# Optimization experiments

Hardware: AMD Instinct MI355X
Metric: run time of the kernel (lower is better)

## Reference

```python
import jax, jax.numpy as jnp
import numpy as np

EMBED_DIM = 1024
NUM_HEADS = 16
HEAD_DIM = EMBED_DIM // NUM_HEADS


def setup_inputs() -> dict:
    key = jax.random.key(0)
    ks = jax.random.split(key, 11)
    B, S, D = 2, 2048, EMBED_DIM
    s = 1.0 / np.sqrt(D)
    inp = {
        "query": jax.random.normal(ks[0], (B, S, D), jnp.float32),
        "key": jax.random.normal(ks[1], (B, S, D), jnp.float32),
        "value": jax.random.normal(ks[2], (B, S, D), jnp.float32),
        # torch Linear weights: [out, in]
        "Wq": jax.random.normal(ks[3], (D, D), jnp.float32) * s,
        "bq": jnp.zeros((D,), jnp.float32),
        "Wk": jax.random.normal(ks[4], (D, D), jnp.float32) * s,
        "bk": jnp.zeros((D,), jnp.float32),
        "Wv": jax.random.normal(ks[5], (D, D), jnp.float32) * s,
        "bv": jnp.zeros((D,), jnp.float32),
        "Wo": jax.random.normal(ks[6], (D, D), jnp.float32) * s,
        "bo": jnp.zeros((D,), jnp.float32),
    }
    return inp


def reference(query, key, value, Wq, bq, Wk, bk, Wv, bv, Wo, bo):
    B, Q, D = query.shape
    K = key.shape[1]
    H, Hd = NUM_HEADS, HEAD_DIM
    # NOTE: source divides by scaling = head_dim**-0.5, i.e. multiplies by sqrt(head_dim)
    scaling = float(Hd) ** (-0.5)

    q = (query @ Wq.T + bq).reshape(B, Q, H, Hd).transpose(0, 2, 1, 3)  # [B,H,Q,Hd]
    k = (key @ Wk.T + bk).reshape(B, K, H, Hd).transpose(0, 2, 1, 3)    # [B,H,K,Hd]
    v = (value @ Wv.T + bv).reshape(B, K, H, Hd).transpose(0, 2, 1, 3)  # [B,H,K,Hd]

    scores = jnp.einsum("bhqd,bhkd->bhqk", q, k) / scaling
    attn = jax.nn.softmax(scores, axis=-1)  # dropout=0 (eval)
    out = jnp.einsum("bhqk,bhkd->bhqd", attn, v)
    out = out.transpose(0, 2, 1, 3).reshape(B, Q, D)
    return out @ Wo.T + bo
```

## Files before the change

kernel.cpp:

```cpp
#include <hip/hip_runtime.h>
#include <type_traits>
#include <utility>

#define B_ 2
#define S_ 2048
#define D_ 1024
#define H_ 16
#define HD_ 64
#define KDIM 1024

typedef __attribute__((ext_vector_type(8))) short    s16x8;
typedef __attribute__((ext_vector_type(8))) _Float16 h16x8;
typedef __attribute__((ext_vector_type(4))) float    f32x4;
typedef __attribute__((ext_vector_type(4))) int      i32x4;
typedef __attribute__((ext_vector_type(2))) int      i32x2;

template <typename T, typename = void> struct mfma_takes : std::false_type {};
template <typename T>
struct mfma_takes<T, std::void_t<decltype(__builtin_amdgcn_mfma_f32_16x16x32_f16(
    std::declval<T>(), std::declval<T>(), std::declval<f32x4>(), 0, 0, 0))>>
    : std::true_type {};
using frag8 = std::conditional_t<mfma_takes<h16x8>::value, h16x8, s16x8>;

__device__ __forceinline__ f32x4 mfma_f16(frag8 a, frag8 b, f32x4 c) {
  return __builtin_amdgcn_mfma_f32_16x16x32_f16(a, b, c, 0, 0, 0);
}

__device__ __forceinline__ short f2h(float f) {
  _Float16 h = (_Float16)f;
  short s; __builtin_memcpy(&s, &h, 2);
  return s;
}
__device__ __forceinline__ int pk2h(float a, float b) {
  auto p = __builtin_amdgcn_cvt_pkrtz(a, b);
  int r; __builtin_memcpy(&r, &p, 4); return r;
}
__device__ __forceinline__ frag8 ld_frag(const short* p) {
  return __builtin_bit_cast(frag8, *(const i32x4*)p);
}
__device__ __forceinline__ float fast_exp2(float x) {
  return __builtin_amdgcn_exp2f(x);
}

typedef __attribute__((address_space(1))) const void gvoid;
typedef __attribute__((address_space(3))) void lvoid;
__device__ __forceinline__ void async_copy16(const void* g, void* l) {
  __builtin_amdgcn_global_load_lds((gvoid*)g, (lvoid*)l, 16, 0, 0);
}

#define RAW_BARRIER() asm volatile("s_barrier" ::: "memory")
#define WAITCNT_VM(n) asm volatile("s_waitcnt vmcnt(" #n ")" ::: "memory")

__global__ __launch_bounds__(256)
void conv_all(const float* __restrict__ q, const float* __restrict__ k,
              const float* __restrict__ v, const float* __restrict__ Wq,
              const float* __restrict__ Wk, const float* __restrict__ Wv,
              const float* __restrict__ Wo,
              short* __restrict__ qh, short* __restrict__ kh,
              short* __restrict__ vh, short* __restrict__ wq,
              short* __restrict__ wk, short* __restrict__ wv,
              short* __restrict__ wo) {
  const int blk = blockIdx.x;
  const float* src; short* dst; int base;
  if (blk < 2048)      { src = q;  dst = qh; base = blk; }
  else if (blk < 4096) { src = k;  dst = kh; base = blk - 2048; }
  else if (blk < 6144) { src = v;  dst = vh; base = blk - 4096; }
  else if (blk < 6656) { src = Wq; dst = wq; base = blk - 6144; }
  else if (blk < 7168) { src = Wk; dst = wk; base = blk - 6656; }
  else if (blk < 7680) { src = Wv; dst = wv; base = blk - 7168; }
  else                 { src = Wo; dst = wo; base = blk - 7680; }
  const int i = base * 2048 + threadIdx.x * 8;
  float4 a0 = *(const float4*)(src + i);
  float4 a1 = *(const float4*)(src + i + 4);
  short h[8] = { f2h(a0.x), f2h(a0.y), f2h(a0.z), f2h(a0.w),
                 f2h(a1.x), f2h(a1.y), f2h(a1.z), f2h(a1.w) };
  i32x4 ph; __builtin_memcpy(&ph, h, 16);
  *(i32x4*)(dst + i) = ph;
}

__global__ __launch_bounds__(256, 3)
void gemm_qkv(const short* __restrict__ qh, const short* __restrict__ kh,
              const short* __restrict__ vh, const short* __restrict__ wq,
              const short* __restrict__ wk, const short* __restrict__ wv,
              const float* __restrict__ bq, const float* __restrict__ bk,
              const float* __restrict__ bv, short* __restrict__ Qf,
              short* __restrict__ Kf, short* __restrict__ Vt, float QS) {
  __shared__ short As[2 * 4096];
  __shared__ short Bs[2 * 4096];

  const int blk = blockIdx.x;
  const int bn = blk & 7, g = blk >> 3;
  const int z = g >> 5, bm = g & 31;
  const short* Ap = z == 0 ? qh : z == 1 ? kh : vh;
  const short* Wp = z == 0 ? wq : z == 1 ? wk : wv;
  const float* bias = z == 0 ? bq : z == 1 ? bk : bv;
  short* Out = z == 0 ? Qf : z == 1 ? Kf : Vt;
  const float scale = z == 0 ? QS : 1.0f;
  const int omode = z == 2 ? 2 : 1;

  const int t = threadIdx.x, wave = t >> 6, lane = t & 63;
  const int laneN = lane & 15, quad = lane >> 4;
  const int wm = wave & 1, wn = wave >> 1;

  f32x4 acc[4][4];
#pragma unroll
  for (int i = 0; i < 4; ++i)
#pragma unroll
    for (int j = 0; j < 4; ++j)
#pragma unroll
      for (int r = 0; r < 4; ++r) acc[i][j][r] = 0.f;

  auto stage = [&](int buf, int kk) {
#pragma unroll
    for (int j = 0; j < 2; ++j) {
      const int chunk = j * 256 + t;
      const int row = chunk >> 2;
      const int gg = (chunk & 3) ^ ((row >> 1) & 3);
      async_copy16(Ap + (size_t)(bm * 128 + row) * KDIM + kk + gg * 8,
                   As + buf * 4096 + chunk * 8);
      async_copy16(Wp + (size_t)(bn * 128 + row) * KDIM + kk + gg * 8,
                   Bs + buf * 4096 + chunk * 8);
    }
  };

  stage(0, 0);
  int buf = 0;
  for (int kk = 0; kk < KDIM; kk += 32, buf ^= 1) {
    if (kk + 32 < KDIM) {
      stage(buf ^ 1, kk + 32);
      WAITCNT_VM(4);
    } else {
      WAITCNT_VM(0);
    }
    RAW_BARRIER();

    frag8 aF[4], bF[4];
#pragma unroll
    for (int mi = 0; mi < 4; ++mi) {
      const int row = wm * 64 + mi * 16 + laneN;
      aF[mi] = ld_frag(As + buf * 4096 + row * 32 +
                       ((quad ^ ((row >> 1) & 3)) * 8));
    }
#pragma unroll
    for (int ni = 0; ni < 4; ++ni) {
      const int row = wn * 64 + ni * 16 + laneN;
      bF[ni] = ld_frag(Bs + buf * 4096 + row * 32 +
                       ((quad ^ ((row >> 1) & 3)) * 8));
    }
#pragma unroll
    for (int mi = 0; mi < 4; ++mi)
#pragma unroll
      for (int ni = 0; ni < 4; ++ni)
        acc[mi][ni] = mfma_f16(aF[mi], bF[ni], acc[mi][ni]);
    RAW_BARRIER();
  }

#pragma unroll
  for (int mi = 0; mi < 4; ++mi)
#pragma unroll
    for (int ni = 0; ni < 4; ++ni) {
      const int colg = bn * 128 + wn * 64 + ni * 16 + laneN;
      const float bb = bias[colg];
      if (omode == 2) {
        const int rowg0 = bm * 128 + wm * 64 + mi * 16 + quad * 4;
        const int b = rowg0 >> 11, s0 = rowg0 & 2047;
        const int h = colg >> 6, hd = colg & 63;
        short pk[4];
#pragma unroll
        for (int r = 0; r < 4; ++r) pk[r] = f2h(acc[mi][ni][r] + bb);
        i32x2 w; __builtin_memcpy(&w, pk, 8);
        *(i32x2*)(Vt + (((size_t)(b * H_ + h)) * HD_ + hd) * S_ + s0) = w;
      } else {
#pragma unroll
        for (int r = 0; r < 4; ++r) {
          const int rowg = bm * 128 + wm * 64 + mi * 16 + quad * 4 + r;
          const int b = rowg >> 11, s = rowg & 2047;
          const int h = colg >> 6, hd = colg & 63;
          Out[(((size_t)(b * H_ + h)) * S_ + s) * HD_ + hd] =
              f2h((acc[mi][ni][r] + bb) * scale);
        }
      }
    }
}

__global__ __launch_bounds__(256, 3)
void gemm_out(const short* __restrict__ Ap, const short* __restrict__ Wp,
              const float* __restrict__ bias, float* __restrict__ Out) {
  __shared__ short As[2 * 4096];
  __shared__ short Bs[2 * 2048];
  const int blk = blockIdx.x;
  const int g = blk >> 3;
  const int bn = (blk & 7) * 2 + (g & 1), bm = g >> 1;

  const int t = threadIdx.x, wave = t >> 6, lane = t & 63;
  const int laneN = lane & 15, quad = lane >> 4;
  const int wm = wave & 1, wn = wave >> 1;

  f32x4 acc[4][2];
#pragma unroll
  for (int i = 0; i < 4; ++i)
#pragma unroll
    for (int j = 0; j < 2; ++j)
#pragma unroll
      for (int r = 0; r < 4; ++r) acc[i][j][r] = 0.f;

  auto stage = [&](int buf, int kk) {
#pragma unroll
    for (int j = 0; j < 2; ++j) {
      const int chunk = j * 256 + t;
      const int row = chunk >> 2;
      const int gg = (chunk & 3) ^ ((row >> 1) & 3);
      async_copy16(Ap + (size_t)(bm * 128 + row) * KDIM + kk + gg * 8,
                   As + buf * 4096 + chunk * 8);
    }
    {
      const int chunk = t;
      const int row = chunk >> 2;
      const int gg = (chunk & 3) ^ ((row >> 1) & 3);
      async_copy16(Wp + (size_t)(bn * 64 + row) * KDIM + kk + gg * 8,
                   Bs + buf * 2048 + chunk * 8);
    }
  };

  stage(0, 0);
  int buf = 0;
  for (int kk = 0; kk < KDIM; kk += 32, buf ^= 1) {
    if (kk + 32 < KDIM) {
      stage(buf ^ 1, kk + 32);
      WAITCNT_VM(3);
    } else {
      WAITCNT_VM(0);
    }
    RAW_BARRIER();

    frag8 aF[4], bF[2];
#pragma unroll
    for (int mi = 0; mi < 4; ++mi) {
      const int row = wm * 64 + mi * 16 + laneN;
      aF[mi] = ld_frag(As + buf * 4096 + row * 32 +
                       ((quad ^ ((row >> 1) & 3)) * 8));
    }
#pragma unroll
    for (int ni = 0; ni < 2; ++ni) {
      const int row = wn * 32 + ni * 16 + laneN;
      bF[ni] = ld_frag(Bs + buf * 2048 + row * 32 +
                       ((quad ^ ((row >> 1) & 3)) * 8));
    }
#pragma unroll
    for (int mi = 0; mi < 4; ++mi)
#pragma unroll
      for (int ni = 0; ni < 2; ++ni)
        acc[mi][ni] = mfma_f16(aF[mi], bF[ni], acc[mi][ni]);
    RAW_BARRIER();
  }

#pragma unroll
  for (int mi = 0; mi < 4; ++mi)
#pragma unroll
    for (int ni = 0; ni < 2; ++ni) {
      const int colg = bn * 64 + wn * 32 + ni * 16 + laneN;
      const float bb = bias[colg];
#pragma unroll
      for (int r = 0; r < 4; ++r) {
        const int rowg = bm * 128 + wm * 64 + mi * 16 + quad * 4 + r;
        Out[(size_t)rowg * 1024 + colg] = acc[mi][ni][r] + bb;
      }
    }
}

__global__ __launch_bounds__(256, 2)
void attn(const short* __restrict__ Qf, const short* __restrict__ Kf,
          const short* __restrict__ Vt_, short* __restrict__ Ow) {
  __shared__ short Ks[2 * 4096];
  __shared__ short Vts[2 * 4096];
  __shared__ short Ps[4][16 * 72];

  const int blk = blockIdx.x;
  const int xcd = blk & 7, local = blk >> 3;
  const int pair = xcd * 4 + (local >> 4);
  const int h = pair & 15, b = pair >> 4, qt = local & 15;
  const size_t head = ((size_t)b * H_ + h) * (size_t)S_ * HD_;

  const int t = threadIdx.x;
  const int wave = t >> 6, lane = t & 63;
  const int laneN = lane & 15, quad = lane >> 4;

  frag8 qf[2][2];
#pragma unroll
  for (int st = 0; st < 2; ++st) {
    const size_t row = (size_t)qt * 128 + wave * 32 + st * 16 + laneN;
#pragma unroll
    for (int half = 0; half < 2; ++half)
      qf[st][half] = ld_frag(Qf + head + row * HD_ + half * 32 + quad * 8);
  }

  f32x4 o[2][4];
  float m_r[2] = { -1e30f, -1e30f }, l_r[2] = { 0.f, 0.f };
#pragma unroll
  for (int st = 0; st < 2; ++st)
#pragma unroll
    for (int i = 0; i < 4; ++i)
#pragma unroll
      for (int j = 0; j < 4; ++j) o[st][i][j] = 0.f;

  auto stage = [&](int buf, int kt) {
#pragma unroll
    for (int j = 0; j < 2; ++j) {
      const int chunk = j * 256 + t;
      const int row = chunk >> 3;
      const int g = (chunk & 7) ^ (row & 7);
      const int ldsoff = buf * 4096 + chunk * 8;
      async_copy16(Kf + head + (size_t)(kt * 64 + row) * HD_ + g * 8, Ks + ldsoff);
      async_copy16(Vt_ + head + (size_t)row * S_ + kt * 64 + g * 8, Vts + ldsoff);
    }
  };

  stage(0, 0);
  int buf = 0;
  for (int kt = 0; kt < 32; ++kt, buf ^= 1) {
    if (kt + 1 < 32) {
      stage(buf ^ 1, kt + 1);
      WAITCNT_VM(4);
    } else {
      WAITCNT_VM(0);
    }
    RAW_BARRIER();

    frag8 vf[4][2];
#pragma unroll
    for (int dt = 0; dt < 4; ++dt) {
      const int row = dt * 16 + laneN;
#pragma unroll
      for (int half = 0; half < 2; ++half)
        vf[dt][half] = ld_frag(Vts + buf * 4096 + row * 64 +
                               (((half * 4 + quad) ^ (row & 7)) * 8));
    }

    f32x4 s[2][4];
#pragma unroll
    for (int nt = 0; nt < 4; ++nt) {
      const int row = nt * 16 + laneN;
      const int o0 = buf * 4096 + row * 64 + ((quad ^ (row & 7)) * 8);
      const int o1 = buf * 4096 + row * 64 + (((quad + 4) ^ (row & 7)) * 8);
      frag8 k0 = ld_frag(Ks + o0), k1 = ld_frag(Ks + o1);
#pragma unroll
      for (int st = 0; st < 2; ++st) {
        f32x4 acc;
#pragma unroll
        for (int j = 0; j < 4; ++j) acc[j] = 0.f;
        acc = mfma_f16(k0, qf[st][0], acc);
        acc = mfma_f16(k1, qf[st][1], acc);
        s[st][nt] = acc;
      }
    }

#pragma unroll
    for (int st = 0; st < 2; ++st) {
      float mx = -1e30f;
#pragma unroll
      for (int nt = 0; nt < 4; ++nt)
#pragma unroll
        for (int r = 0; r < 4; ++r) mx = fmaxf(mx, s[st][nt][r]);
      mx = fmaxf(mx, __shfl_xor(mx, 16));
      mx = fmaxf(mx, __shfl_xor(mx, 32));
      const float mold = m_r[st];
      const float mn = fmaxf(mold, mx);
      float rs = 0.f;
#pragma unroll
      for (int nt = 0; nt < 4; ++nt)
#pragma unroll
        for (int r = 0; r < 4; ++r) {
          const float p = fast_exp2(s[st][nt][r] - mn);
          s[st][nt][r] = p; rs += p;
        }
      rs += __shfl_xor(rs, 16);
      rs += __shfl_xor(rs, 32);
      if (__any(mn > mold)) {
        const float al = fast_exp2(mold - mn);
        m_r[st] = mn;
        l_r[st] = l_r[st] * al + rs;
#pragma unroll
        for (int dt = 0; dt < 4; ++dt)
#pragma unroll
          for (int r = 0; r < 4; ++r) o[st][dt][r] *= al;
      } else {
        l_r[st] += rs;
      }

#pragma unroll
      for (int nt = 0; nt < 4; ++nt) {
        i32x2 w;
        w[0] = pk2h(s[st][nt][0], s[st][nt][1]);
        w[1] = pk2h(s[st][nt][2], s[st][nt][3]);
        *(i32x2*)&Ps[wave][laneN * 72 + nt * 16 + quad * 4] = w;
      }
      const frag8 p0 = ld_frag(&Ps[wave][laneN * 72 + quad * 8]);
      const frag8 p1 = ld_frag(&Ps[wave][laneN * 72 + 32 + quad * 8]);
#pragma unroll
      for (int dt = 0; dt < 4; ++dt) {
        o[st][dt] = mfma_f16(vf[dt][0], p0, o[st][dt]);
        o[st][dt] = mfma_f16(vf[dt][1], p1, o[st][dt]);
      }
    }
    RAW_BARRIER();
  }

#pragma unroll
  for (int st = 0; st < 2; ++st) {
    const float inv = 1.0f / l_r[st];
    const int sg = qt * 128 + wave * 32 + st * 16 + laneN;
    short* dst = Ow + ((size_t)b * S_ + sg) * D_ + h * HD_;
#pragma unroll
    for (int dt = 0; dt < 4; ++dt) {
      short pk[4] = { f2h(o[st][dt][0] * inv), f2h(o[st][dt][1] * inv),
                      f2h(o[st][dt][2] * inv), f2h(o[st][dt][3] * inv) };
      i32x2 w; __builtin_memcpy(&w, pk, 8);
      *(i32x2*)(dst + dt * 16 + quad * 4) = w;
    }
  }
}

extern "C" void kernel_launch(void* const* d_in, const int* in_sizes, int n_in,
                              void* d_out, int out_size, void* d_ws, size_t ws_size,
                              hipStream_t stream) {
  const float* q  = (const float*)d_in[0];
  const float* k  = (const float*)d_in[1];
  const float* v  = (const float*)d_in[2];
  const float* Wq = (const float*)d_in[3];
  const float* bq = (const float*)d_in[4];
  const float* Wk = (const float*)d_in[5];
  const float* bk = (const float*)d_in[6];
  const float* Wv = (const float*)d_in[7];
  const float* bv = (const float*)d_in[8];
  const float* Wo = (const float*)d_in[9];
  const float* bo = (const float*)d_in[10];

  const size_t NTOK = (size_t)B_ * S_ * D_;
  const size_t NW   = (size_t)D_ * D_;
  short* p = (short*)d_ws;
  short* qh = p; p += NTOK;  short* kh = p; p += NTOK;  short* vh = p; p += NTOK;
  short* wq = p; p += NW;    short* wk = p; p += NW;
  short* wv = p; p += NW;    short* wo = p; p += NW;
  short* Qf = p; p += NTOK;  short* Kf = p; p += NTOK;
  short* Vt = p; p += NTOK;  short* Ow = p; p += NTOK;

  dim3 blk(256);

  conv_all<<<8192, blk, 0, stream>>>(q, k, v, Wq, Wk, Wv, Wo,
                                     qh, kh, vh, wq, wk, wv, wo);

  const float QS = 11.541560327111707f;
  gemm_qkv<<<768, blk, 0, stream>>>(qh, kh, vh, wq, wk, wv, bq, bk, bv,
                                    Qf, Kf, Vt, QS);

  attn<<<512, blk, 0, stream>>>(Qf, Kf, Vt, Ow);

  gemm_out<<<512, blk, 0, stream>>>(Ow, wo, bo, (float*)d_out);
}
```

Baseline: 231.4 us.

## Triple-buffer GEMM pipelines and split attention across 8 waves

Both projection GEMMs move from a double-buffered to a triple-buffered LDS pipeline, prefetching two K-steps ahead so global loads have more time to land before they are consumed. The attention kernel doubles its block to 512 threads, with each wave owning 16 query rows instead of 32. That halves per-wave registers and MFMA work and spreads the K/V staging loads over more threads. The costs are more LDS per GEMM block, which may cut occupancy, and the attention K/V tile loads are amortized over fewer query rows per wave.

```diff
diff --git a/kernel.cpp b/kernel.cpp
--- a/kernel.cpp
+++ b/kernel.cpp
@@ -85,8 +85,8 @@
               const float* __restrict__ bq, const float* __restrict__ bk,
               const float* __restrict__ bv, short* __restrict__ Qf,
               short* __restrict__ Kf, short* __restrict__ Vt, float QS) {
-  __shared__ short As[2 * 4096];
-  __shared__ short Bs[2 * 4096];
+  __shared__ short As[3 * 4096];
+  __shared__ short Bs[3 * 4096];
 
   const int blk = blockIdx.x;
   const int bn = blk & 7, g = blk >> 3;
@@ -124,10 +124,14 @@
   };
 
   stage(0, 0);
+  stage(1, 32);
   int buf = 0;
-  for (int kk = 0; kk < KDIM; kk += 32, buf ^= 1) {
-    if (kk + 32 < KDIM) {
-      stage(buf ^ 1, kk + 32);
+  for (int kk = 0; kk < KDIM; kk += 32) {
+    if (kk + 64 < KDIM) {
+      int nb = buf + 2; if (nb >= 3) nb -= 3;
+      stage(nb, kk + 64);
+      WAITCNT_VM(8);
+    } else if (kk + 32 < KDIM) {
       WAITCNT_VM(4);
     } else {
       WAITCNT_VM(0);
@@ -153,6 +157,7 @@
       for (int ni = 0; ni < 4; ++ni)
         acc[mi][ni] = mfma_f16(aF[mi], bF[ni], acc[mi][ni]);
     RAW_BARRIER();
+    buf = buf + 1 == 3 ? 0 : buf + 1;
   }
 
 #pragma unroll
@@ -186,8 +191,8 @@
 __global__ __launch_bounds__(256, 3)
 void gemm_out(const short* __restrict__ Ap, const short* __restrict__ Wp,
               const float* __restrict__ bias, float* __restrict__ Out) {
-  __shared__ short As[2 * 4096];
-  __shared__ short Bs[2 * 2048];
+  __shared__ short As[3 * 4096];
+  __shared__ short Bs[3 * 2048];
   const int blk = blockIdx.x;
   const int g = blk >> 3;
   const int bn = (blk & 7) * 2 + (g & 1), bm = g >> 1;
@@ -223,10 +228,14 @@
   };
 
   stage(0, 0);
+  stage(1, 32);
   int buf = 0;
-  for (int kk = 0; kk < KDIM; kk += 32, buf ^= 1) {
-    if (kk + 32 < KDIM) {
-      stage(buf ^ 1, kk + 32);
+  for (int kk = 0; kk < KDIM; kk += 32) {
+    if (kk + 64 < KDIM) {
+      int nb = buf + 2; if (nb >= 3) nb -= 3;
+      stage(nb, kk + 64);
+      WAITCNT_VM(6);
+    } else if (kk + 32 < KDIM) {
       WAITCNT_VM(3);
     } else {
       WAITCNT_VM(0);
@@ -252,6 +261,7 @@
       for (int ni = 0; ni < 2; ++ni)
         acc[mi][ni] = mfma_f16(aF[mi], bF[ni], acc[mi][ni]);
     RAW_BARRIER();
+    buf = buf + 1 == 3 ? 0 : buf + 1;
   }
 
 #pragma unroll
@@ -268,12 +278,12 @@
     }
 }
 
-__global__ __launch_bounds__(256, 2)
+__global__ __launch_bounds__(512, 2)
 void attn(const short* __restrict__ Qf, const short* __restrict__ Kf,
           const short* __restrict__ Vt_, short* __restrict__ Ow) {
   __shared__ short Ks[2 * 4096];
   __shared__ short Vts[2 * 4096];
-  __shared__ short Ps[4][16 * 72];
+  __shared__ short Ps[8][16 * 72];
 
   const int blk = blockIdx.x;
   const int xcd = blk & 7, local = blk >> 3;
@@ -285,34 +295,28 @@
   const int wave = t >> 6, lane = t & 63;
   const int laneN = lane & 15, quad = lane >> 4;
 
-  frag8 qf[2][2];
-#pragma unroll
-  for (int st = 0; st < 2; ++st) {
-    const size_t row = (size_t)qt * 128 + wave * 32 + st * 16 + laneN;
+  frag8 qf[2];
+  {
+    const size_t row = (size_t)qt * 128 + wave * 16 + laneN;
 #pragma unroll
     for (int half = 0; half < 2; ++half)
-      qf[st][half] = ld_frag(Qf + head + row * HD_ + half * 32 + quad * 8);
+      qf[half] = ld_frag(Qf + head + row * HD_ + half * 32 + quad * 8);
   }
 
-  f32x4 o[2][4];
-  float m_r[2] = { -1e30f, -1e30f }, l_r[2] = { 0.f, 0.f };
-#pragma unroll
-  for (int st = 0; st < 2; ++st)
-#pragma unroll
-    for (int i = 0; i < 4; ++i)
-#pragma unroll
-      for (int j = 0; j < 4; ++j) o[st][i][j] = 0.f;
+  f32x4 o[4];
+  float m_r = -1e30f, l_r = 0.f;
+#pragma unroll
+  for (int i = 0; i < 4; ++i)
+#pragma unroll
+    for (int j = 0; j < 4; ++j) o[i][j] = 0.f;
 
   auto stage = [&](int buf, int kt) {
-#pragma unroll
-    for (int j = 0; j < 2; ++j) {
-      const int chunk = j * 256 + t;
-      const int row = chunk >> 3;
-      const int g = (chunk & 7) ^ (row & 7);
-      const int ldsoff = buf * 4096 + chunk * 8;
-      async_copy16(Kf + head + (size_t)(kt * 64 + row) * HD_ + g * 8, Ks + ldsoff);
-      async_copy16(Vt_ + head + (size_t)row * S_ + kt * 64 + g * 8, Vts + ldsoff);
-    }
+    const int chunk = t;
+    const int row = chunk >> 3;
+    const int g = (chunk & 7) ^ (row & 7);
+    const int ldsoff = buf * 4096 + chunk * 8;
+    async_copy16(Kf + head + (size_t)(kt * 64 + row) * HD_ + g * 8, Ks + ldsoff);
+    async_copy16(Vt_ + head + (size_t)row * S_ + kt * 64 + g * 8, Vts + ldsoff);
   };
 
   stage(0, 0);
@@ -320,7 +324,7 @@
   for (int kt = 0; kt < 32; ++kt, buf ^= 1) {
     if (kt + 1 < 32) {
       stage(buf ^ 1, kt + 1);
-      WAITCNT_VM(4);
+      WAITCNT_VM(2);
     } else {
       WAITCNT_VM(0);
     }
@@ -336,84 +340,79 @@
                                (((half * 4 + quad) ^ (row & 7)) * 8));
     }
 
-    f32x4 s[2][4];
+    f32x4 s[4];
 #pragma unroll
     for (int nt = 0; nt < 4; ++nt) {
       const int row = nt * 16 + laneN;
       const int o0 = buf * 4096 + row * 64 + ((quad ^ (row & 7)) * 8);
       const int o1 = buf * 4096 + row * 64 + (((quad + 4) ^ (row & 7)) * 8);
       frag8 k0 = ld_frag(Ks + o0), k1 = ld_frag(Ks + o1);
-#pragma unroll
-      for (int st = 0; st < 2; ++st) {
-        f32x4 acc;
-#pragma unroll
-        for (int j = 0; j < 4; ++j) acc[j] = 0.f;
-        acc = mfma_f16(k0, qf[st][0], acc);
-        acc = mfma_f16(k1, qf[st][1], acc);
-        s[st][nt] = acc;
-      }
-    }
-
-#pragma unroll
-    for (int st = 0; st < 2; ++st) {
+      f32x4 acc;
+#pragma unroll
+      for (int j = 0; j < 4; ++j) acc[j] = 0.f;
+      acc = mfma_f16(k0, qf[0], acc);
+      acc = mfma_f16(k1, qf[1], acc);
+      s[nt] = acc;
+    }
+
+    {
       float mx = -1e30f;
 #pragma unroll
       for (int nt = 0; nt < 4; ++nt)
 #pragma unroll
-        for (int r = 0; r < 4; ++r) mx = fmaxf(mx, s[st][nt][r]);
+        for (int r = 0; r < 4; ++r) mx = fmaxf(mx, s[nt][r]);
       mx = fmaxf(mx, __shfl_xor(mx, 16));
       mx = fmaxf(mx, __shfl_xor(mx, 32));
-      const float mold = m_r[st];
+      const float mold = m_r;
       const float mn = fmaxf(mold, mx);
       float rs = 0.f;
 #pragma unroll
       for (int nt = 0; nt < 4; ++nt)
 #pragma unroll
         for (int r = 0; r < 4; ++r) {
-          const float p = fast_exp2(s[st][nt][r] - mn);
-          s[st][nt][r] = p; rs += p;
+          const float p = fast_exp2(s[nt][r] - mn);
+          s[nt][r] = p; rs += p;
         }
       rs += __shfl_xor(rs, 16);
       rs += __shfl_xor(rs, 32);
       if (__any(mn > mold)) {
         const float al = fast_exp2(mold - mn);
-        m_r[st] = mn;
-        l_r[st] = l_r[st] * al + rs;
+        m_r = mn;
+        l_r = l_r * al + rs;
 #pragma unroll
         for (int dt = 0; dt < 4; ++dt)
 #pragma unroll
-          for (int r = 0; r < 4; ++r) o[st][dt][r] *= al;
+          for (int r = 0; r < 4; ++r) o[dt][r] *= al;
       } else {
-        l_r[st] += rs;
+        l_r += rs;
       }
-
-#pragma unroll
-      for (int nt = 0; nt < 4; ++nt) {
-        i32x2 w;
-        w[0] = pk2h(s[st][nt][0], s[st][nt][1]);
-        w[1] = pk2h(s[st][nt][2], s[st][nt][3]);
-        *(i32x2*)&Ps[wave][laneN * 72 + nt * 16 + quad * 4] = w;
-      }
-      const frag8 p0 = ld_frag(&Ps[wave][laneN * 72 + quad * 8]);
-      const frag8 p1 = ld_frag(&Ps[wave][laneN * 72 + 32 + quad * 8]);
-#pragma unroll
-      for (int dt = 0; dt < 4; ++dt) {
-        o[st][dt] = mfma_f16(vf[dt][0], p0, o[st][dt]);
-        o[st][dt] = mfma_f16(vf[dt][1], p1, o[st][dt]);
-      }
+    }
+
+#pragma unroll
+    for (int nt = 0; nt < 4; ++nt) {
+      i32x2 w;
+      w[0] = pk2h(s[nt][0], s[nt][1]);
+      w[1] = pk2h(s[nt][2], s[nt][3]);
+      *(i32x2*)&Ps[wave][laneN * 72 + nt * 16 + quad * 4] = w;
+    }
+    const frag8 p0 = ld_frag(&Ps[wave][laneN * 72 + quad * 8]);
+    const frag8 p1 = ld_frag(&Ps[wave][laneN * 72 + 32 + quad * 8]);
+#pragma unroll
+    for (int dt = 0; dt < 4; ++dt) {
+      o[dt] = mfma_f16(vf[dt][0], p0, o[dt]);
+      o[dt] = mfma_f16(vf[dt][1], p1, o[dt]);
     }
     RAW_BARRIER();
   }
 
-#pragma unroll
-  for (int st = 0; st < 2; ++st) {
-    const float inv = 1.0f / l_r[st];
-    const int sg = qt * 128 + wave * 32 + st * 16 + laneN;
+  {
+    const float inv = 1.0f / l_r;
+    const int sg = qt * 128 + wave * 16 + laneN;
     short* dst = Ow + ((size_t)b * S_ + sg) * D_ + h * HD_;
 #pragma unroll
     for (int dt = 0; dt < 4; ++dt) {
-      short pk[4] = { f2h(o[st][dt][0] * inv), f2h(o[st][dt][1] * inv),
-                      f2h(o[st][dt][2] * inv), f2h(o[st][dt][3] * inv) };
+      short pk[4] = { f2h(o[dt][0] * inv), f2h(o[dt][1] * inv),
+                      f2h(o[dt][2] * inv), f2h(o[dt][3] * inv) };
       i32x2 w; __builtin_memcpy(&w, pk, 8);
       *(i32x2*)(dst + dt * 16 + quad * 4) = w;
     }
@@ -453,7 +452,7 @@
   gemm_qkv<<<768, blk, 0, stream>>>(qh, kh, vh, wq, wk, wv, bq, bk, bv,
                                     Qf, Kf, Vt, QS);
 
-  attn<<<512, blk, 0, stream>>>(Qf, Kf, Vt, Ow);
+  attn<<<512, dim3(512), 0, stream>>>(Qf, Kf, Vt, Ow);
 
   gemm_out<<<512, blk, 0, stream>>>(Ow, wo, bo, (float*)d_out);
 }
```

After: 227.7 us. About the same (-1.6%).
